# Kernel tuning notes

Measured on AMD Instinct MI355X. Metric: run time of the kernel, lower is better.

The kernel has to match this reference:

```python
import jax, jax.numpy as jnp
import numpy as np

LEN = 4          # self.lenth: 4x4 window grid -> max seq len 16
HEADS = 16
SHIFT = LEN // 2 # cyclic shift of lenth//2 in generate_mask


def _build_mask(n):
    # generate_mask(h=heads//2, w=2, p=LEN, shift=SHIFT), type != 'W'
    h, w, p = HEADS // 2, 2, LEN
    s = p - SHIFT
    m = np.zeros((h, w, p, p, p, p), dtype=bool)
    m[-1, :, :s, :, s:, :] = True
    m[-1, :, s:, :, :s, :] = True
    m[:, -1, :, :s, :, s:] = True
    m[:, -1, :, s:, :, :s] = True
    # 'w1 w2 p1 p2 p3 p4 -> 1 (w1 w2) (p1 p2) (p3 p4)' (contiguous merge)
    m = m.reshape(1, h * w, p * p, p * p)
    return jnp.asarray(m[:, :, :n, :n])


def _rel_indices(n):
    cord = np.array([[i, j] for i in range(LEN) for j in range(LEN)])  # (16,2)
    rel = cord[:n, None, :] - cord[None, :n, :] + LEN - 1              # (n,n,2)
    return rel[..., 0], rel[..., 1]


def setup_inputs() -> dict:
    key = jax.random.key(0)
    ks = jax.random.split(key, 6)
    b, n, dim = 4096, 16, 512
    inner = HEADS * 64  # heads * dim_head = 1024
    return {
        "x": jax.random.normal(ks[0], (b, n, dim), dtype=jnp.float32),
        "w_qkv": jax.random.normal(ks[1], (3 * inner, dim), dtype=jnp.float32) * 0.02,
        "b_qkv": jax.random.normal(ks[2], (3 * inner,), dtype=jnp.float32) * 0.02,
        "w_proj": jax.random.normal(ks[3], (dim, inner), dtype=jnp.float32) * 0.02,
        "b_proj": jax.random.normal(ks[4], (dim,), dtype=jnp.float32) * 0.02,
        "rel_pos": jax.random.normal(ks[5], (HEADS, 2 * LEN - 1, 2 * LEN - 1), dtype=jnp.float32) * 0.02,
    }


def reference(x, w_qkv, b_qkv, w_proj, b_proj, rel_pos):
    b, n, _ = x.shape
    h = HEADS
    # type != 'W' -> cyclic shift along tokens
    x = jnp.roll(x, -(n // 2), axis=1)
    qkv = x @ w_qkv.T + b_qkv                       # (b, n, 3*inner)
    q, k, v = jnp.split(qkv, 3, axis=-1)
    split = lambda t: t.reshape(b, n, h, -1).transpose(0, 2, 1, 3)  # b h n d
    q, k, v = split(q), split(k), split(v)
    scale = q.shape[-1] ** -0.5
    dots = jnp.einsum('bhid,bhjd->bhij', q, k) * scale
    r0, r1 = _rel_indices(n)
    dots = dots + rel_pos[:, r0, r1][None]          # (1, h, n, n) rel-pos bias
    mask = _build_mask(n)                           # (1, h, n, n) bool
    dots = jnp.where(mask, -jnp.inf, dots)
    attn = jax.nn.softmax(dots, axis=-1)
    out = jnp.einsum('bhij,bhjd->bhid', attn, v)
    out = out.transpose(0, 2, 1, 3).reshape(b, n, -1)  # (b, n, inner)
    return out @ w_proj.T + b_proj
```

## Files before the change

### kernel.cpp

```cpp
#include <hip/hip_runtime.h>
#include <stdint.h>


typedef __attribute__((ext_vector_type(8))) short frag8;
typedef __attribute__((ext_vector_type(4))) float frag4f;

__device__ __forceinline__ uint16_t f2bf(float f) {
  union { float f; uint32_t i; } x; x.f = f;
  uint32_t r = x.i + 0x7fffu + ((x.i >> 16) & 1u);
  return (uint16_t)(r >> 16);
}


__global__ __launch_bounds__(256)
void k_cvt(const float* __restrict__ src, uint16_t* __restrict__ dst, int n4, int ok)
{
  if (!ok) return;
  int i = blockIdx.x * 256 + threadIdx.x;
  const int stride = gridDim.x * 256;
  for (; i < n4; i += stride) {
    float4 v = ((const float4*)src)[i];
    ushort4 o;
    o.x = f2bf(v.x); o.y = f2bf(v.y); o.z = f2bf(v.z); o.w = f2bf(v.w);
    ((ushort4*)dst)[i] = o;
  }
}


struct SmemGemm { uint16_t A[128 * 32]; uint16_t B[192 * 32]; };
struct SmemEpi  { uint16_t q[128][72]; uint16_t k[128][72];
                  uint16_t vT[64][136]; uint16_t p[8][16][24]; };
union Smem1 { SmemGemm s; SmemEpi e; };

__global__ __launch_bounds__(256, 2)
void k_qkv_attn(const uint16_t* __restrict__ xb, const uint16_t* __restrict__ wqkvb,
                const float* __restrict__ b_qkv, const float* __restrict__ rel_pos,
                uint16_t* __restrict__ attn16, int ws_ok)
{
  __shared__ Smem1 sm;
  const int bid  = blockIdx.x;
  const int h    = bid & 15;
  const int mt   = bid >> 4;
  const int t    = threadIdx.x;
  const int lane = t & 63;
  const int wv   = t >> 6;
  const int l15  = lane & 15;
  const int quad = lane >> 4;
  const int wr   = wv & 1;
  const int wc   = wv >> 1;

  if (!ws_ok) {
    #pragma unroll
    for (int i = 0; i < 32; ++i) {
      const int local = t + 256 * i;
      const int row = local >> 6, col = local & 63;
      attn16[(mt * 128 + row) * 1024 + h * 64 + col] = 0;
    }
    return;
  }

  const int arow0 = t >> 2, aoff = t & 3;
  const int g0 = mt * 128 + arow0;
  const int g1 = g0 + 64;
  const int asrc0 = (((g0 & ~15) | ((g0 + 8) & 15)) * 512) + aoff * 8;
  const int asrc1 = (((g1 & ~15) | ((g1 + 8) & 15)) * 512) + aoff * 8;
  int bsrc[3];
  #pragma unroll
  for (int i = 0; i < 3; ++i) {
    int c = t + 256 * i;
    int brow = c >> 2;
    int gc = (brow < 64) ? (h * 64 + brow)
           : (brow < 128) ? (1024 + h * 64 + (brow - 64))
                          : (2048 + h * 64 + (brow - 128));
    bsrc[i] = gc * 512 + (c & 3) * 8;
  }

  frag4f acc[4][6];
  #pragma unroll
  for (int a = 0; a < 4; ++a)
    #pragma unroll
    for (int b = 0; b < 6; ++b) acc[a][b] = (frag4f)0.0f;

  for (int kk = 0; kk < 16; ++kk) {
    const int kb = kk * 32;
    uint4 va0 = *(const uint4*)(xb + asrc0 + kb);
    uint4 va1 = *(const uint4*)(xb + asrc1 + kb);
    uint4 vb0 = *(const uint4*)(wqkvb + bsrc[0] + kb);
    uint4 vb1 = *(const uint4*)(wqkvb + bsrc[1] + kb);
    uint4 vb2 = *(const uint4*)(wqkvb + bsrc[2] + kb);
    __syncthreads();
    *(uint4*)&sm.s.A[t * 8]         = va0;
    *(uint4*)&sm.s.A[(t + 256) * 8] = va1;
    *(uint4*)&sm.s.B[t * 8]         = vb0;
    *(uint4*)&sm.s.B[(t + 256) * 8] = vb1;
    *(uint4*)&sm.s.B[(t + 512) * 8] = vb2;
    __syncthreads();
    frag8 af[4], bf[6];
    #pragma unroll
    for (int rt = 0; rt < 4; ++rt)
      af[rt] = *(const frag8*)&sm.s.A[(wr * 64 + rt * 16 + l15) * 32 + quad * 8];
    #pragma unroll
    for (int ct = 0; ct < 6; ++ct)
      bf[ct] = *(const frag8*)&sm.s.B[((wc * 6 + ct) * 16 + l15) * 32 + quad * 8];
    #pragma unroll
    for (int rt = 0; rt < 4; ++rt)
      #pragma unroll
      for (int ct = 0; ct < 6; ++ct)
        acc[rt][ct] = __builtin_amdgcn_mfma_f32_16x16x32_bf16(af[rt], bf[ct], acc[rt][ct], 0, 0, 0);
  }
  __syncthreads();

  #pragma unroll
  for (int ct = 0; ct < 6; ++ct) {
    const int C = (wc * 6 + ct) * 16 + l15;
    const int gc = (C < 64) ? (h * 64 + C)
                 : (C < 128) ? (1024 + h * 64 + (C - 64))
                             : (2048 + h * 64 + (C - 128));
    const float bias = b_qkv[gc];
    #pragma unroll
    for (int rt = 0; rt < 4; ++rt) {
      #pragma unroll
      for (int r = 0; r < 4; ++r) {
        const int row = wr * 64 + rt * 16 + quad * 4 + r;
        const uint16_t val = f2bf(acc[rt][ct][r] + bias);
        if (C < 64)       sm.e.q[row][C] = val;
        else if (C < 128) sm.e.k[row][C - 64] = val;
        else              sm.e.vT[C - 128][row] = val;
      }
    }
  }
  __syncthreads();

  const float scl = 0.125f;
  #pragma unroll
  for (int bbi = 0; bbi < 2; ++bbi) {
    const int bb = wv * 2 + bbi;
    frag8 a0 = *(const frag8*)&sm.e.q[bb * 16 + l15][quad * 8];
    frag8 a1 = *(const frag8*)&sm.e.q[bb * 16 + l15][32 + quad * 8];
    frag8 b0 = *(const frag8*)&sm.e.k[bb * 16 + l15][quad * 8];
    frag8 b1 = *(const frag8*)&sm.e.k[bb * 16 + l15][32 + quad * 8];
    frag4f s = (frag4f)0.0f;
    s = __builtin_amdgcn_mfma_f32_16x16x32_bf16(a0, b0, s, 0, 0, 0);
    s = __builtin_amdgcn_mfma_f32_16x16x32_bf16(a1, b1, s, 0, 0, 0);
    const int j = l15;
    #pragma unroll
    for (int r = 0; r < 4; ++r) {
      const int i = quad * 4 + r;
      const int r0 = (i >> 2) - (j >> 2) + 3;
      const int r1 = (i & 3) - (j & 3) + 3;
      const float bias = rel_pos[h * 49 + r0 * 7 + r1];
      const bool msk = ((h >= 14) && (((i >> 2) < 2) != ((j >> 2) < 2))) ||
                       ((h & 1)  && (((i & 3) < 2) != ((j & 3) < 2)));
      float v = msk ? -1e30f : (s[r] * scl + bias);
      float m = v;
      m = fmaxf(m, __shfl_xor(m, 1));
      m = fmaxf(m, __shfl_xor(m, 2));
      m = fmaxf(m, __shfl_xor(m, 4));
      m = fmaxf(m, __shfl_xor(m, 8));
      float e = __expf(v - m);
      float su = e;
      su += __shfl_xor(su, 1);
      su += __shfl_xor(su, 2);
      su += __shfl_xor(su, 4);
      su += __shfl_xor(su, 8);
      sm.e.p[bb][i][j] = f2bf(e / su);
    }
  }
  __syncthreads();

  #pragma unroll
  for (int bbi = 0; bbi < 2; ++bbi) {
    const int bb = wv * 2 + bbi;
    frag8 ap;
    if (quad < 2) ap = *(const frag8*)&sm.e.p[bb][l15][quad * 8];
    else          ap = (frag8)0;
    #pragma unroll
    for (int dt = 0; dt < 4; ++dt) {
      frag8 bv = *(const frag8*)&sm.e.vT[dt * 16 + l15][bb * 16 + (quad & 1) * 8];
      frag4f o = (frag4f)0.0f;
      o = __builtin_amdgcn_mfma_f32_16x16x32_bf16(ap, bv, o, 0, 0, 0);
      #pragma unroll
      for (int r = 0; r < 4; ++r) {
        const int grow = mt * 128 + bb * 16 + quad * 4 + r;
        attn16[grow * 1024 + h * 64 + dt * 16 + l15] = f2bf(o[r]);
      }
    }
  }
}


__global__ __launch_bounds__(512, 4)
void k_proj(const uint16_t* __restrict__ attn16, const uint16_t* __restrict__ wprojb,
            const float* __restrict__ b_proj, float* __restrict__ out, int ws_ok)
{
  __shared__ uint8_t smraw[2 * 36864];
  const int mt   = blockIdx.x;
  const int t    = threadIdx.x;
  const int lane = t & 63;
  const int wv   = t >> 6;
  const int l15  = lane & 15;
  const int quad = lane >> 4;

  if (!ws_ok) {
    for (int i = t; i < 64 * 512; i += 512) {
      const int row = i >> 9, col = i & 511;
      out[(mt * 64 + row) * 512 + col] = b_proj[col];
    }
    return;
  }

  const int cnt = (wv < 4) ? 5 : 4;
  const int c0  = (wv < 4) ? wv * 5 : 20 + (wv - 4) * 4;

  const uint16_t* gp[5];
  int lds_off[5];
  #pragma unroll
  for (int o = 0; o < 5; ++o) {
    int c = c0 + o;
    if (c > 35) c = 35;
    const int e = c * 512 + lane * 8;
    if (e < 2048) {
      gp[o] = attn16 + (size_t)(mt * 64 + (e >> 5)) * 1024 + (e & 31);
    } else {
      const int eb = e - 2048;
      gp[o] = wprojb + (size_t)(eb >> 5) * 1024 + (eb & 31);
    }
    lds_off[o] = (c0 + o) * 1024;
  }

  frag4f acc[4][4];
  #pragma unroll
  for (int a = 0; a < 4; ++a)
    #pragma unroll
    for (int b = 0; b < 4; ++b) acc[a][b] = (frag4f)0.0f;

  auto STAGE = [&](int buf, int kk) {
    #pragma unroll
    for (int o = 0; o < 5; ++o)
      if (o < cnt)
        __builtin_amdgcn_global_load_lds(
            (const __attribute__((address_space(1))) void*)(gp[o] + kk * 32),
            (__attribute__((address_space(3))) void*)(smraw + buf * 36864 + lds_off[o]),
            16, 0, 0);
  };

  STAGE(0, 0);
  __syncthreads();

  for (int kk = 0; kk < 32; ++kk) {
    const int cur = kk & 1;
    if (kk < 31) STAGE(cur ^ 1, kk + 1);

    const uint16_t* As = (const uint16_t*)(smraw + cur * 36864);
    const uint16_t* Bs = (const uint16_t*)(smraw + cur * 36864 + 4096);
    frag8 af[4];
    #pragma unroll
    for (int rt = 0; rt < 4; ++rt)
      af[rt] = *(const frag8*)(As + (rt * 16 + l15) * 32 + quad * 8);
    #pragma unroll
    for (int ct = 0; ct < 4; ++ct) {
      frag8 bfr = *(const frag8*)(Bs + (wv * 64 + ct * 16 + l15) * 32 + quad * 8);
      #pragma unroll
      for (int rt = 0; rt < 4; ++rt)
        acc[rt][ct] = __builtin_amdgcn_mfma_f32_16x16x32_bf16(af[rt], bfr, acc[rt][ct], 0, 0, 0);
    }
    __syncthreads();
  }

  #pragma unroll
  for (int ct = 0; ct < 4; ++ct) {
    const int gcol = wv * 64 + ct * 16 + l15;
    const float bias = b_proj[gcol];
    #pragma unroll
    for (int rt = 0; rt < 4; ++rt) {
      #pragma unroll
      for (int r = 0; r < 4; ++r) {
        const int grow = mt * 64 + rt * 16 + quad * 4 + r;
        out[grow * 512 + gcol] = acc[rt][ct][r] + bias;
      }
    }
  }
}


extern "C" void kernel_launch(void* const* d_in, const int* in_sizes, int n_in,
                              void* d_out, int out_size, void* d_ws, size_t ws_size,
                              hipStream_t stream) {
  const float* x      = (const float*)d_in[0];
  const float* w_qkv  = (const float*)d_in[1];
  const float* b_qkv  = (const float*)d_in[2];
  const float* w_proj = (const float*)d_in[3];
  const float* b_proj = (const float*)d_in[4];
  const float* rel    = (const float*)d_in[5];

  uint16_t* xb     = (uint16_t*)d_ws;
  uint16_t* wqkvb  = xb + 33554432;
  uint16_t* wprojb = wqkvb + 1572864;
  const size_t ws_need = (size_t)(33554432 + 1572864 + 524288) * 2;
  const int ws_ok = (ws_size >= ws_need) ? 1 : 0;

  uint16_t* attn16 = (uint16_t*)d_out;
  float*    out    = (float*)d_out;

  k_cvt<<<dim3(4096), dim3(256), 0, stream>>>(x,      xb,     33554432 / 4, ws_ok);
  k_cvt<<<dim3(1536), dim3(256), 0, stream>>>(w_qkv,  wqkvb,  1572864 / 4,  ws_ok);
  k_cvt<<<dim3(512),  dim3(256), 0, stream>>>(w_proj, wprojb, 524288 / 4,   ws_ok);
  k_qkv_attn<<<dim3(512 * 16), dim3(256), 0, stream>>>(xb, wqkvb, b_qkv, rel, attn16, ws_ok);
  k_proj    <<<dim3(1024),     dim3(512), 0, stream>>>(attn16, wprojb, b_proj, out, ws_ok);
}
```

Before: 672.4 us.

## Double-buffer QKV GEMM with direct global-to-LDS loads and XOR-swizzled LDS

```diff
diff --git a/kernel.cpp b/kernel.cpp
--- a/kernel.cpp
+++ b/kernel.cpp
@@ -27,10 +27,9 @@
 }
 
 
-struct SmemGemm { uint16_t A[128 * 32]; uint16_t B[192 * 32]; };
 struct SmemEpi  { uint16_t q[128][72]; uint16_t k[128][72];
                   uint16_t vT[64][136]; uint16_t p[8][16][24]; };
-union Smem1 { SmemGemm s; SmemEpi e; };
+union Smem1 { uint8_t g[2][20480]; SmemEpi e; };
 
 __global__ __launch_bounds__(256, 2)
 void k_qkv_attn(const uint16_t* __restrict__ xb, const uint16_t* __restrict__ wqkvb,
@@ -59,20 +58,25 @@
     return;
   }
 
-  const int arow0 = t >> 2, aoff = t & 3;
-  const int g0 = mt * 128 + arow0;
-  const int g1 = g0 + 64;
-  const int asrc0 = (((g0 & ~15) | ((g0 + 8) & 15)) * 512) + aoff * 8;
-  const int asrc1 = (((g1 & ~15) | ((g1 + 8) & 15)) * 512) + aoff * 8;
-  int bsrc[3];
-  #pragma unroll
-  for (int i = 0; i < 3; ++i) {
-    int c = t + 256 * i;
-    int brow = c >> 2;
-    int gc = (brow < 64) ? (h * 64 + brow)
-           : (brow < 128) ? (1024 + h * 64 + (brow - 64))
-                          : (2048 + h * 64 + (brow - 128));
-    bsrc[i] = gc * 512 + (c & 3) * 8;
+  const int slot_g = (lane & 3) ^ ((lane >> 3) & 3);
+  const uint16_t* sp[5];
+  int ldsoff[5];
+  #pragma unroll
+  for (int o = 0; o < 5; ++o) {
+    const int c = wv * 5 + o;
+    const int rloc = c * 16 + (lane >> 2);
+    if (c < 8) {
+      const int g = mt * 128 + rloc;
+      const int srow = (g & ~15) | ((g + 8) & 15);
+      sp[o] = xb + srow * 512 + slot_g * 8;
+    } else {
+      const int cb = rloc - 128;
+      const int gc = (cb < 64) ? (h * 64 + cb)
+                   : (cb < 128) ? (1024 + h * 64 + (cb - 64))
+                                : (2048 + h * 64 + (cb - 128));
+      sp[o] = wqkvb + gc * 512 + slot_g * 8;
+    }
+    ldsoff[o] = c * 1024;
   }
 
   frag4f acc[4][6];
@@ -81,34 +85,38 @@
     #pragma unroll
     for (int b = 0; b < 6; ++b) acc[a][b] = (frag4f)0.0f;
 
+  auto STAGE = [&](int buf, int kk) {
+    #pragma unroll
+    for (int o = 0; o < 5; ++o)
+      __builtin_amdgcn_global_load_lds(
+          (const __attribute__((address_space(1))) void*)(sp[o] + kk * 32),
+          (__attribute__((address_space(3))) void*)(sm.g[buf] + ldsoff[o]),
+          16, 0, 0);
+  };
+
+  STAGE(0, 0);
+  __syncthreads();
+
+  const int xq = quad ^ ((l15 >> 1) & 3);
   for (int kk = 0; kk < 16; ++kk) {
-    const int kb = kk * 32;
-    uint4 va0 = *(const uint4*)(xb + asrc0 + kb);
-    uint4 va1 = *(const uint4*)(xb + asrc1 + kb);
-    uint4 vb0 = *(const uint4*)(wqkvb + bsrc[0] + kb);
-    uint4 vb1 = *(const uint4*)(wqkvb + bsrc[1] + kb);
-    uint4 vb2 = *(const uint4*)(wqkvb + bsrc[2] + kb);
-    __syncthreads();
-    *(uint4*)&sm.s.A[t * 8]         = va0;
-    *(uint4*)&sm.s.A[(t + 256) * 8] = va1;
-    *(uint4*)&sm.s.B[t * 8]         = vb0;
-    *(uint4*)&sm.s.B[(t + 256) * 8] = vb1;
-    *(uint4*)&sm.s.B[(t + 512) * 8] = vb2;
-    __syncthreads();
+    const int cur = kk & 1;
+    if (kk < 15) STAGE(cur ^ 1, kk + 1);
+
+    const uint8_t* base = sm.g[cur];
     frag8 af[4], bf[6];
     #pragma unroll
     for (int rt = 0; rt < 4; ++rt)
-      af[rt] = *(const frag8*)&sm.s.A[(wr * 64 + rt * 16 + l15) * 32 + quad * 8];
+      af[rt] = *(const frag8*)(base + (wr * 64 + rt * 16 + l15) * 64 + xq * 16);
     #pragma unroll
     for (int ct = 0; ct < 6; ++ct)
-      bf[ct] = *(const frag8*)&sm.s.B[((wc * 6 + ct) * 16 + l15) * 32 + quad * 8];
+      bf[ct] = *(const frag8*)(base + 8192 + ((wc * 6 + ct) * 16 + l15) * 64 + xq * 16);
     #pragma unroll
     for (int rt = 0; rt < 4; ++rt)
       #pragma unroll
       for (int ct = 0; ct < 6; ++ct)
         acc[rt][ct] = __builtin_amdgcn_mfma_f32_16x16x32_bf16(af[rt], bf[ct], acc[rt][ct], 0, 0, 0);
-  }
-  __syncthreads();
+    __syncthreads();
+  }
 
   #pragma unroll
   for (int ct = 0; ct < 6; ++ct) {
@@ -211,6 +219,7 @@
 
   const int cnt = (wv < 4) ? 5 : 4;
   const int c0  = (wv < 4) ? wv * 5 : 20 + (wv - 4) * 4;
+  const int slot_g = (lane & 3) ^ ((lane >> 3) & 3);
 
   const uint16_t* gp[5];
   int lds_off[5];
@@ -218,12 +227,11 @@
   for (int o = 0; o < 5; ++o) {
     int c = c0 + o;
     if (c > 35) c = 35;
-    const int e = c * 512 + lane * 8;
-    if (e < 2048) {
-      gp[o] = attn16 + (size_t)(mt * 64 + (e >> 5)) * 1024 + (e & 31);
+    const int rloc = c * 16 + (lane >> 2);
+    if (c < 4) {
+      gp[o] = attn16 + (size_t)(mt * 64 + rloc) * 1024 + slot_g * 8;
     } else {
-      const int eb = e - 2048;
-      gp[o] = wprojb + (size_t)(eb >> 5) * 1024 + (eb & 31);
+      gp[o] = wprojb + (size_t)(rloc - 64) * 1024 + slot_g * 8;
     }
     lds_off[o] = (c0 + o) * 1024;
   }
@@ -247,6 +255,7 @@
   STAGE(0, 0);
   __syncthreads();
 
+  const int xq = quad ^ ((l15 >> 1) & 3);
   for (int kk = 0; kk < 32; ++kk) {
     const int cur = kk & 1;
     if (kk < 31) STAGE(cur ^ 1, kk + 1);
@@ -256,10 +265,10 @@
     frag8 af[4];
     #pragma unroll
     for (int rt = 0; rt < 4; ++rt)
-      af[rt] = *(const frag8*)(As + (rt * 16 + l15) * 32 + quad * 8);
+      af[rt] = *(const frag8*)(As + (rt * 16 + l15) * 32 + xq * 8);
     #pragma unroll
     for (int ct = 0; ct < 4; ++ct) {
-      frag8 bfr = *(const frag8*)(Bs + (wv * 64 + ct * 16 + l15) * 32 + quad * 8);
+      frag8 bfr = *(const frag8*)(Bs + (wv * 64 + ct * 16 + l15) * 32 + xq * 8);
       #pragma unroll
       for (int rt = 0; rt < 4; ++rt)
         acc[rt][ct] = __builtin_amdgcn_mfma_f32_16x16x32_bf16(af[rt], bfr, acc[rt][ct], 0, 0, 0);
```

Measured after the change: 633.7 us. 5.7% less time.
